# Kernel tuning notes

Hardware: AMD Instinct MI355X
Metric: run time of the kernel (lower is better)

The kernel has to match this reference:

```python
import jax, jax.numpy as jnp
import numpy as np

K = 5            # spline kernel size per dim
NUM_CLASSES = 10
EPS = 1e-4       # matches module's normalize eps
ROUTING_ITERS = 3
_BITS = jnp.array([[(b >> 2) & 1, (b >> 1) & 1, b & 1] for b in range(8)], dtype=jnp.float32)  # [8,3]


def normalize(t, axis=-1):
    return t / (jnp.sqrt(jnp.sum(t * t, axis=axis, keepdims=True)) + EPS)


def quat_mul(q, r):
    # quaternions stored (x, y, z, w) -- module sets identity as [:,:,:,3]=1
    qx, qy, qz, qw = q[..., 0], q[..., 1], q[..., 2], q[..., 3]
    rx, ry, rz, rw = r[..., 0], r[..., 1], r[..., 2], r[..., 3]
    return jnp.stack([
        qw * rx + qx * rw + qy * rz - qz * ry,
        qw * ry - qx * rz + qy * rw + qz * rx,
        qw * rz + qx * ry - qy * rx + qz * rw,
        qw * rw - qx * rx - qy * ry - qz * rz,
    ], axis=-1)


def spline_conv(x, pseudo, src, dst, W, root, bias, n_nodes):
    # degree-1 open B-spline conv, kernel 5^3, in=1, out=16
    v = pseudo * (K - 1)                                   # [E,3]
    i0 = jnp.clip(jnp.floor(v), 0, K - 2)                  # [E,3]
    frac = v - i0
    i0 = i0.astype(jnp.int32)
    idx = i0[:, None, :] + _BITS.astype(jnp.int32)[None]   # [E,8,3]
    kflat = (idx[..., 0] * K + idx[..., 1]) * K + idx[..., 2]  # [E,8]
    wb = jnp.prod(jnp.where(_BITS[None] > 0, frac[:, None, :], 1.0 - frac[:, None, :]), axis=-1)  # [E,8]
    Wg = W[kflat]                                          # [E,8,16] irregular gather (dominant traffic)
    wk = jnp.einsum('eb,ebo->eo', wb, Wg)                  # [E,16]
    msg = x[src] * wk                                      # [E,16] (in-channels = 1)
    agg = jax.ops.segment_sum(msg, dst, num_segments=n_nodes)
    deg = jax.ops.segment_sum(jnp.ones_like(dst, dtype=x.dtype), dst, num_segments=n_nodes)
    return agg / jnp.maximum(deg, 1.0)[:, None] + x @ root + bias


def caps_layer(pose, act, q):
    # pose [N,I,4], act [N,I], q [I,J,4] -> pose [N,J,4], act [N,J]
    qn = normalize(q)
    pred = normalize(quat_mul(qn[None], pose[:, :, None, :]))  # [N,I,J,4]
    b = jnp.zeros(pred.shape[:3], dtype=pose.dtype)
    for _ in range(ROUTING_ITERS):
        c = jax.nn.softmax(b, axis=2) * act[:, :, None]
        s = jnp.einsum('nij,nijq->njq', c, pred)
        v = normalize(s)
        b = b + jnp.einsum('nijq,njq->nij', pred, v)
    act_out = jax.nn.sigmoid(jnp.einsum('nij,nijq,njq->nj', c, pred, v))
    return v, act_out


def pool_by_agreement(pose, act, pos, G, start, size):
    # voxel-grid clustering + agreement-weighted quaternion averaging
    g = jnp.clip(jnp.floor((pos - start) / size), 0, G - 1).astype(jnp.int32)  # [N,3]
    vid = (g[:, 0] * G + g[:, 1]) * G + g[:, 2]
    V = G ** 3
    s = jax.ops.segment_sum(act[:, :, None] * pose, vid, num_segments=V)  # [V,J,4]
    m = normalize(s)
    agree = jnp.sum(pose * m[vid], axis=-1)                                # [N,J]
    wsum = jax.ops.segment_sum(act, vid, num_segments=V)
    cnt = jax.ops.segment_sum(jnp.ones((pose.shape[0],), pose.dtype), vid, num_segments=V)
    act_out = jax.nn.sigmoid(jax.ops.segment_sum(act * agree, vid, num_segments=V) / (wsum + EPS))
    pos_out = jax.ops.segment_sum(pos, vid, num_segments=V) / (cnt[:, None] + EPS)
    return m, act_out, pos_out


def forward(x, pos, pseudo, W_spline, root, bias, lin_w, lin_b, q0, q1, q3, q5, q6, q7, edge_index):
    N = x.shape[0]
    src, dst = edge_index[0], edge_index[1]
    h = spline_conv(x, pseudo, src, dst, W_spline, root, bias, N)   # [N,16]
    quats = jax.nn.elu(h) @ lin_w + lin_b                           # [N,4]
    pose = normalize(quats.reshape(N, 1, 4))                        # [N,1,4]
    act = x.reshape(N, 1)                                           # expand to num_caps_in=1
    pose, act = caps_layer(pose, act, q0)                           # 1 -> 6
    pose, act = caps_layer(pose, act, q1)                           # 6 -> 6
    min_pos, max_pos = pos.min(), pos.max()
    rng = max_pos + 0.001 - min_pos
    pose, act, p = pool_by_agreement(pose, act, pos, 32, min_pos, rng / 32)   # -> 32768 voxels
    pose, act = caps_layer(pose, act, q3)                           # 6 -> 8
    pose, act, p = pool_by_agreement(pose, act, p, 8, min_pos, rng / 8)       # -> 512
    pose, act = caps_layer(pose, act, q5)                           # 8 -> 12
    pose, act, p = pool_by_agreement(pose, act, p, 2, min_pos, rng / 2)       # -> 8
    pose, act = caps_layer(pose, act, q6)                           # 12 -> 14
    pose, act, p = pool_by_agreement(pose, act, p, 1, min_pos - 0.5, max_pos - min_pos + 1.0)  # -> 1
    pose, act = caps_layer(pose, act, q7)                           # 14 -> 10
    return act                                                      # [1, 10]


def setup_inputs() -> dict:
    key = jax.random.key(0)
    ks = jax.random.split(key, 16)
    N, E = 50000, 800000
    def caps_q(k, i, j):
        return jax.random.normal(k, (i, j, 4), dtype=jnp.float32)
    return {
        'x': jax.random.uniform(ks[0], (N, 1), dtype=jnp.float32),
        'pos': jax.random.uniform(ks[1], (N, 3), dtype=jnp.float32),
        'pseudo': jax.random.uniform(ks[2], (E, 3), dtype=jnp.float32),
        'W_spline': jax.random.normal(ks[3], (K ** 3, 16), dtype=jnp.float32) * 0.1,
        'root': jax.random.normal(ks[4], (1, 16), dtype=jnp.float32) * 0.1,
        'bias': jnp.zeros((16,), dtype=jnp.float32),
        'lin_w': jax.random.normal(ks[5], (16, 4), dtype=jnp.float32) * 0.25,
        'lin_b': jnp.zeros((4,), dtype=jnp.float32),
        'q0': caps_q(ks[6], 1, 6),
        'q1': caps_q(ks[7], 6, 6),
        'q3': caps_q(ks[8], 6, 8),
        'q5': caps_q(ks[9], 8, 12),
        'q6': caps_q(ks[10], 12, 14),
        'q7': caps_q(ks[11], 14, NUM_CLASSES),
        'edge_index': jax.random.randint(ks[12], (2, E), 0, N, dtype=jnp.int32),
    }


def reference(x, pos, pseudo, W_spline, root, bias, lin_w, lin_b, q0, q1, q3, q5, q6, q7, edge_index):
    return forward(x, pos, pseudo, W_spline, root, bias, lin_w, lin_b, q0, q1, q3, q5, q6, q7, edge_index)
```

## Files before the change

kernel.cpp:

```cpp
#include <hip/hip_runtime.h>
#include <math.h>

#define EPS 1e-4f

__device__ __forceinline__ float sigmoidf_(float x){ return 1.0f/(1.0f+expf(-x)); }

__device__ __forceinline__ unsigned f2u_(float f){
    unsigned u = __float_as_uint(f);
    return (u & 0x80000000u) ? ~u : (u | 0x80000000u);
}
__device__ __forceinline__ float u2f_(unsigned u){
    unsigned b = (u & 0x80000000u) ? (u & 0x7FFFFFFFu) : ~u;
    return __uint_as_float(b);
}

__global__ void init_kernel(unsigned* __restrict__ mm, int* __restrict__ deg, int N,
                            int* __restrict__ vhead, int V,
                            float* __restrict__ pz, int PZ){
    int i = blockIdx.x*blockDim.x + threadIdx.x;
    int stride = gridDim.x*blockDim.x;
    if (i == 0){ mm[0] = 0xFFFFFFFFu; mm[1] = 0u; }
    for (int t = i; t < N; t += stride) deg[t] = 0;
    for (int t = i; t < V; t += stride) vhead[t] = -1;
    for (int t = i; t < PZ; t += stride) pz[t] = 0.f;
}

__global__ void prep_kernel(const float* __restrict__ p, int n3, unsigned* mm,
                            const int* __restrict__ ei, int* __restrict__ deg,
                            int* __restrict__ rank, int E){
    int gid = blockIdx.x*blockDim.x + threadIdx.x;
    int stride = gridDim.x*blockDim.x;
    float lo = INFINITY, hi = -INFINITY;
    for (int i = gid; i < n3; i += stride){
        float v = p[i]; lo = fminf(lo, v); hi = fmaxf(hi, v);
    }
    for (int off = 32; off > 0; off >>= 1){
        lo = fminf(lo, __shfl_down(lo, off));
        hi = fmaxf(hi, __shfl_down(hi, off));
    }
    __shared__ float slo[4], shi[4];
    int wid = threadIdx.x >> 6;
    if ((threadIdx.x & 63) == 0){ slo[wid] = lo; shi[wid] = hi; }
    __syncthreads();
    if (threadIdx.x == 0){
        for (int w = 1; w < 4; w++){ lo = fminf(lo, slo[w]); hi = fmaxf(hi, shi[w]); }
        atomicMin(&mm[0], f2u_(lo));
        atomicMax(&mm[1], f2u_(hi));
    }
    for (int e = gid; e < E; e += stride)
        rank[e] = atomicAdd(&deg[ei[E + e]], 1);
}

__global__ __launch_bounds__(256)
void scan_bsum(const int* __restrict__ deg, int* __restrict__ bsum, int N){
    int i = blockIdx.x*256 + threadIdx.x;
    int v = (i < N) ? deg[i] : 0;
    for (int o = 32; o > 0; o >>= 1) v += __shfl_down(v, o);
    __shared__ int ws[4];
    if ((threadIdx.x & 63) == 0) ws[threadIdx.x >> 6] = v;
    __syncthreads();
    if (threadIdx.x == 0) bsum[blockIdx.x] = ws[0] + ws[1] + ws[2] + ws[3];
}

__global__ __launch_bounds__(1024)
void scan_top(int* __restrict__ bsum, int NB){
    __shared__ int sh[1024];
    int t = threadIdx.x;
    int v = (t < NB) ? bsum[t] : 0;
    sh[t] = v;
    __syncthreads();
    for (int d = 1; d < 1024; d <<= 1){
        int u = (t >= d) ? sh[t - d] : 0;
        __syncthreads();
        sh[t] += u;
        __syncthreads();
    }
    if (t < NB) bsum[t] = sh[t] - v;
    if (t == 1023) bsum[NB] = sh[1023];
}

__global__ __launch_bounds__(256)
void scan_final(const int* __restrict__ deg, const int* __restrict__ bsum,
                int* __restrict__ off, int N, int NB){
    __shared__ int sh[256];
    int b = blockIdx.x;
    int i = b*256 + threadIdx.x;
    int v = (i < N) ? deg[i] : 0;
    sh[threadIdx.x] = v;
    __syncthreads();
    for (int d = 1; d < 256; d <<= 1){
        int u = (threadIdx.x >= d) ? sh[threadIdx.x - d] : 0;
        __syncthreads();
        sh[threadIdx.x] += u;
        __syncthreads();
    }
    if (i < N) off[i] = bsum[b] + sh[threadIdx.x] - v;
    if (b == 0 && threadIdx.x == 0) off[N] = bsum[NB];
}

__global__ void edge_pack(const int* __restrict__ ei, const float* __restrict__ pseudo,
                          const float* __restrict__ x,
                          const int* __restrict__ rank, const int* __restrict__ off,
                          float4* __restrict__ rec4, int* __restrict__ recb, int E){
    int e = blockIdx.x*blockDim.x + threadIdx.x;
    if (e >= E) return;
    float p0 = pseudo[3*e], p1 = pseudo[3*e+1], p2 = pseudo[3*e+2];
    int s = ei[e], d = ei[E + e];
    float v0 = p0*4.f, v1 = p1*4.f, v2 = p2*4.f;
    float f0 = fminf(fmaxf(floorf(v0), 0.f), 3.f);
    float f1 = fminf(fmaxf(floorf(v1), 0.f), 3.f);
    float f2 = fminf(fmaxf(floorf(v2), 0.f), 3.f);
    int slot = off[d] + rank[e];
    rec4[slot] = make_float4(v0 - f0, v1 - f1, v2 - f2, x[s]);
    recb[slot] = ((int)f0*5 + (int)f1)*5 + (int)f2;
}

__device__ __forceinline__ int voxel_id(const float* __restrict__ pos, int n, int G,
                                        float start, float size){
    int g[3];
    #pragma unroll
    for (int k = 0; k < 3; k++){
        float gg = floorf((pos[(size_t)n*3 + k] - start) / size);
        gg = fminf(fmaxf(gg, 0.f), (float)(G - 1));
        g[k] = (int)gg;
    }
    return (g[0]*G + g[1])*G + g[2];
}

__device__ __forceinline__ void pool_geom(const unsigned* mm, int G, int mode,
                                          float& start, float& size){
    float mn = u2f_(mm[0]), mx = u2f_(mm[1]);
    if (mode == 0){ start = mn; size = (mx + 0.001f - mn) / (float)G; }
    else          { start = mn - 0.5f; size = mx - mn + 1.0f; }
}

__global__ __launch_bounds__(256)
void spline_node_kernel(const float* __restrict__ x, const float4* __restrict__ rec4,
                        const int* __restrict__ recb, const int* __restrict__ off,
                        const float* __restrict__ W,
                        const float* __restrict__ root, const float* __restrict__ bias,
                        const float* __restrict__ lin_w, const float* __restrict__ lin_b,
                        float* __restrict__ pose, float* __restrict__ act, int N){
    __shared__ float Ws[125*17];
    for (int i = threadIdx.x; i < 125*16; i += blockDim.x)
        Ws[(i >> 4)*17 + (i & 15)] = W[i];
    __syncthreads();
    int t = blockIdx.x*blockDim.x + threadIdx.x;
    int n = t >> 3;
    int k = t & 7;
    if (n >= N) return;

    int o0 = off[n], o1 = off[n+1];

    float agg[16];
    #pragma unroll
    for (int o = 0; o < 16; o++) agg[o] = 0.f;

    for (int s = o0 + k; s < o1; s += 8){
        float4 rv = rec4[s];
        int base = recb[s];
        float fr0 = rv.x, fr1 = rv.y, fr2 = rv.z, xv = rv.w;
        #pragma unroll
        for (int b = 0; b < 8; b++){
            int b0 = (b >> 2) & 1, b1 = (b >> 1) & 1, b2 = b & 1;
            float w = (b0 ? fr0 : 1.f - fr0) * (b1 ? fr1 : 1.f - fr1) * (b2 ? fr2 : 1.f - fr2);
            w *= xv;
            const float* Wr = &Ws[(base + b0*25 + b1*5 + b2)*17];
            #pragma unroll
            for (int o = 0; o < 16; o++) agg[o] += w * Wr[o];
        }
    }

    #pragma unroll
    for (int o = 0; o < 16; o++){
        agg[o] += __shfl_xor(agg[o], 1);
        agg[o] += __shfl_xor(agg[o], 2);
        agg[o] += __shfl_xor(agg[o], 4);
    }

    if (k != 0) return;

    float deg = fmaxf((float)(o1 - o0), 1.0f);
    float xs = x[n];
    float qv0 = lin_b[0], qv1 = lin_b[1], qv2 = lin_b[2], qv3 = lin_b[3];
    #pragma unroll
    for (int o = 0; o < 16; o++){
        float h = agg[o] / deg + xs * root[o] + bias[o];
        float e = (h > 0.f) ? h : expm1f(h);
        qv0 += e * lin_w[o*4 + 0];
        qv1 += e * lin_w[o*4 + 1];
        qv2 += e * lin_w[o*4 + 2];
        qv3 += e * lin_w[o*4 + 3];
    }
    float inv = 1.0f / (sqrtf(qv0*qv0 + qv1*qv1 + qv2*qv2 + qv3*qv3) + EPS);
    pose[(size_t)n*4 + 0] = qv0*inv;
    pose[(size_t)n*4 + 1] = qv1*inv;
    pose[(size_t)n*4 + 2] = qv2*inv;
    pose[(size_t)n*4 + 3] = qv3*inv;
    act[n] = xs;
}

__device__ __forceinline__ void quat_pred(const float* qq, float px, float py, float pz,
                                          float pw, float* pr){
    float qx=qq[0], qy=qq[1], qz=qq[2], qw=qq[3];
    float tx = qw*px + qx*pw + qy*pz - qz*py;
    float ty = qw*py - qx*pz + qy*pw + qz*px;
    float tz = qw*pz + qx*py - qy*px + qz*pw;
    float tw = qw*pw - qx*px - qy*py - qz*pz;
    float inv = 1.f/(sqrtf(tx*tx+ty*ty+tz*tz+tw*tw)+EPS);
    pr[0]=tx*inv; pr[1]=ty*inv; pr[2]=tz*inv; pr[3]=tw*inv;
}

template<int I>
__device__ __forceinline__ void caps_route8(const float (*pr)[4], const float* a, bool on,
                                            float* c, float& v0, float& v1,
                                            float& v2, float& v3){
    float b[I];
    #pragma unroll
    for (int i = 0; i < I; i++) b[i] = on ? 0.f : -INFINITY;
    v0=v1=v2=v3=0.f;
    #pragma unroll
    for (int t = 0; t < 3; t++){
        #pragma unroll
        for (int i = 0; i < I; i++){
            float mb = b[i];
            mb = fmaxf(mb, __shfl_xor(mb, 1));
            mb = fmaxf(mb, __shfl_xor(mb, 2));
            mb = fmaxf(mb, __shfl_xor(mb, 4));
            float e = on ? expf(b[i] - mb) : 0.f;
            float s = e;
            s += __shfl_xor(s, 1);
            s += __shfl_xor(s, 2);
            s += __shfl_xor(s, 4);
            c[i] = a[i] * e / s;
        }
        float s0=0.f, s1=0.f, s2=0.f, s3=0.f;
        #pragma unroll
        for (int i = 0; i < I; i++){
            s0 += c[i]*pr[i][0]; s1 += c[i]*pr[i][1];
            s2 += c[i]*pr[i][2]; s3 += c[i]*pr[i][3];
        }
        float inv = 1.f/(sqrtf(s0*s0+s1*s1+s2*s2+s3*s3)+EPS);
        v0=s0*inv; v1=s1*inv; v2=s2*inv; v3=s3*inv;
        if (t < 2){
            #pragma unroll
            for (int i = 0; i < I; i++)
                b[i] += pr[i][0]*v0 + pr[i][1]*v1 + pr[i][2]*v2 + pr[i][3]*v3;
        }
    }
}

__global__ __launch_bounds__(256)
void caps01_kernel(const float* __restrict__ pose0, const float* __restrict__ act0,
                   const float* __restrict__ q0, const float* __restrict__ q1,
                   float* __restrict__ poseOut, float* __restrict__ actOut,
                   const float* __restrict__ pos, int* __restrict__ vhead,
                   int* __restrict__ vnxt, int N, int G,
                   const unsigned* __restrict__ mm){
    __shared__ float qn0[6*4], qn1[36*4];
    for (int t = threadIdx.x; t < 6; t += blockDim.x){
        float qa=q0[t*4],qb=q0[t*4+1],qc=q0[t*4+2],qd=q0[t*4+3];
        float inv=1.f/(sqrtf(qa*qa+qb*qb+qc*qc+qd*qd)+EPS);
        qn0[t*4]=qa*inv; qn0[t*4+1]=qb*inv; qn0[t*4+2]=qc*inv; qn0[t*4+3]=qd*inv;
    }
    for (int t = threadIdx.x; t < 36; t += blockDim.x){
        float qa=q1[t*4],qb=q1[t*4+1],qc=q1[t*4+2],qd=q1[t*4+3];
        float inv=1.f/(sqrtf(qa*qa+qb*qb+qc*qc+qd*qd)+EPS);
        qn1[t*4]=qa*inv; qn1[t*4+1]=qb*inv; qn1[t*4+2]=qc*inv; qn1[t*4+3]=qd*inv;
    }
    __syncthreads();
    int tid = blockIdx.x*blockDim.x + threadIdx.x;
    int n = tid >> 3, j = tid & 7;
    if (n >= N) return;
    bool on = (j < 6);

    float4 p0 = *reinterpret_cast<const float4*>(&pose0[(size_t)n*4]);
    float aa0[1] = { act0[n] };
    float pr0[1][4] = {{0.f,0.f,0.f,0.f}};
    if (on) quat_pred(&qn0[j*4], p0.x, p0.y, p0.z, p0.w, pr0[0]);
    float c0[1], v0x, v0y, v0z, v0w;
    caps_route8<1>(pr0, aa0, on, c0, v0x, v0y, v0z, v0w);
    float al0 = sigmoidf_(c0[0]*(pr0[0][0]*v0x + pr0[0][1]*v0y
                                + pr0[0][2]*v0z + pr0[0][3]*v0w));

    float pi[6][4], ai[6];
    #pragma unroll
    for (int i = 0; i < 6; i++){
        pi[i][0] = __shfl(v0x, i, 8);
        pi[i][1] = __shfl(v0y, i, 8);
        pi[i][2] = __shfl(v0z, i, 8);
        pi[i][3] = __shfl(v0w, i, 8);
        ai[i]    = __shfl(al0, i, 8);
    }

    float pr[6][4];
    #pragma unroll
    for (int i = 0; i < 6; i++){
        pr[i][0]=pr[i][1]=pr[i][2]=pr[i][3]=0.f;
        if (on) quat_pred(&qn1[(i*6+j)*4], pi[i][0], pi[i][1], pi[i][2], pi[i][3], pr[i]);
    }
    float c1[6], v1x, v1y, v1z, v1w;
    caps_route8<6>(pr, ai, on, c1, v1x, v1y, v1z, v1w);
    if (on){
        float acc = 0.f;
        #pragma unroll
        for (int i = 0; i < 6; i++)
            acc += c1[i]*(pr[i][0]*v1x + pr[i][1]*v1y + pr[i][2]*v1z + pr[i][3]*v1w);
        actOut[(size_t)n*6 + j] = sigmoidf_(acc);
        *reinterpret_cast<float4*>(&poseOut[((size_t)n*6 + j)*4]) =
            make_float4(v1x, v1y, v1z, v1w);
    }
    if (j == 0){
        float start, size; pool_geom(mm, G, 0, start, size);
        int vid = voxel_id(pos, n, G, start, size);
        vnxt[n] = atomicExch(&vhead[vid], n);
    }
}

__global__ __launch_bounds__(256)
void pool1caps_kernel(const float* __restrict__ poseIn, const float* __restrict__ actIn,
                      const float* __restrict__ pos,
                      const int* __restrict__ head, const int* __restrict__ nxt,
                      const float* __restrict__ q3,
                      float* __restrict__ poseOut, float* __restrict__ actOut,
                      float* __restrict__ posOut, int V){
    __shared__ float qn[48*4];
    for (int t = threadIdx.x; t < 48; t += blockDim.x){
        float qa=q3[t*4],qb=q3[t*4+1],qc=q3[t*4+2],qd=q3[t*4+3];
        float inv=1.f/(sqrtf(qa*qa+qb*qb+qc*qc+qd*qd)+EPS);
        qn[t*4]=qa*inv; qn[t*4+1]=qb*inv; qn[t*4+2]=qc*inv; qn[t*4+3]=qd*inv;
    }
    __syncthreads();
    int tid = blockIdx.x*blockDim.x + threadIdx.x;
    int v = tid >> 3, j = tid & 7;
    if (v >= V) return;
    bool onj = (j < 6);

    float s0=0.f,s1=0.f,s2=0.f,s3=0.f, w=0.f, ps0=0.f,ps1=0.f,ps2=0.f;
    int cnt = 0;
    for (int n = head[v]; n >= 0; n = nxt[n]){
        if (onj){
            float aj = actIn[(size_t)n*6 + j];
            float4 pb = *reinterpret_cast<const float4*>(&poseIn[((size_t)n*6 + j)*4]);
            s0 += aj*pb.x; s1 += aj*pb.y; s2 += aj*pb.z; s3 += aj*pb.w;
            w += aj;
        } else if (j == 6){
            ps0 += pos[(size_t)n*3+0]; ps1 += pos[(size_t)n*3+1]; ps2 += pos[(size_t)n*3+2];
        }
        cnt++;
    }
    float m0=0.f,m1=0.f,m2=0.f,m3=0.f;
    if (onj){
        float inv = 1.f/(sqrtf(s0*s0+s1*s1+s2*s2+s3*s3)+EPS);
        m0=s0*inv; m1=s1*inv; m2=s2*inv; m3=s3*inv;
    }
    float ag = 0.f;
    for (int n = head[v]; n >= 0; n = nxt[n]){
        if (onj){
            float aj = actIn[(size_t)n*6 + j];
            float4 pb = *reinterpret_cast<const float4*>(&poseIn[((size_t)n*6 + j)*4]);
            ag += aj*(pb.x*m0 + pb.y*m1 + pb.z*m2 + pb.w*m3);
        }
    }
    float actm = sigmoidf_(ag/(w+EPS));
    if (j == 6){
        float c = (float)cnt + EPS;
        posOut[(size_t)v*3+0] = ps0/c;
        posOut[(size_t)v*3+1] = ps1/c;
        posOut[(size_t)v*3+2] = ps2/c;
    }

    float pi[6][4], ai[6];
    #pragma unroll
    for (int i = 0; i < 6; i++){
        pi[i][0] = __shfl(m0, i, 8);
        pi[i][1] = __shfl(m1, i, 8);
        pi[i][2] = __shfl(m2, i, 8);
        pi[i][3] = __shfl(m3, i, 8);
        ai[i]    = __shfl(actm, i, 8);
    }
    float pr[6][4];
    #pragma unroll
    for (int i = 0; i < 6; i++)
        quat_pred(&qn[(i*8+j)*4], pi[i][0], pi[i][1], pi[i][2], pi[i][3], pr[i]);
    float c1[6], vx, vy, vz, vw;
    caps_route8<6>(pr, ai, true, c1, vx, vy, vz, vw);
    float acc = 0.f;
    #pragma unroll
    for (int i = 0; i < 6; i++)
        acc += c1[i]*(pr[i][0]*vx + pr[i][1]*vy + pr[i][2]*vz + pr[i][3]*vw);
    actOut[(size_t)v*8 + j] = sigmoidf_(acc);
    *reinterpret_cast<float4*>(&poseOut[((size_t)v*8 + j)*4]) = make_float4(vx, vy, vz, vw);
}

template<int V, int J, int CH, int NCHUNK>
__global__ void pool_priv1(const float4* __restrict__ poseIn, const float* __restrict__ actIn,
                           const float* __restrict__ posIn,
                           float* __restrict__ s, float* __restrict__ wsum,
                           float* __restrict__ cnt, float* __restrict__ psum,
                           int N, int G, int mode, const unsigned* __restrict__ mm){
    __shared__ float s_[V*CH*4];
    __shared__ float wsum_[V*CH];
    __shared__ float cnt_[V];
    __shared__ float psum_[V*3];
    const int chunk = blockIdx.x % NCHUNK;
    const int slice = blockIdx.x / NCHUNK;
    const int nslices = gridDim.x / NCHUNK;
    const int c0 = chunk * CH;

    for (int t = threadIdx.x; t < V*CH*4; t += blockDim.x) s_[t] = 0.f;
    for (int t = threadIdx.x; t < V*CH; t += blockDim.x) wsum_[t] = 0.f;
    if (chunk == 0){
        for (int t = threadIdx.x; t < V; t += blockDim.x) cnt_[t] = 0.f;
        for (int t = threadIdx.x; t < V*3; t += blockDim.x) psum_[t] = 0.f;
    }
    __syncthreads();

    float start, size; pool_geom(mm, G, mode, start, size);
    int per = (N + nslices - 1) / nslices;
    int n0 = slice * per, n1 = min(N, n0 + per);

    for (int n = n0 + (int)threadIdx.x; n < n1; n += blockDim.x){
        int vid = voxel_id(posIn, n, G, start, size);
        #pragma unroll
        for (int jj = 0; jj < CH; jj++){
            int j = c0 + jj;
            float aj = actIn[(size_t)n*J + j];
            float4 p = poseIn[(size_t)n*J + j];
            int b = (vid*CH + jj)*4;
            atomicAdd(&s_[b+0], aj*p.x);
            atomicAdd(&s_[b+1], aj*p.y);
            atomicAdd(&s_[b+2], aj*p.z);
            atomicAdd(&s_[b+3], aj*p.w);
            atomicAdd(&wsum_[vid*CH + jj], aj);
        }
        if (chunk == 0){
            atomicAdd(&cnt_[vid], 1.0f);
            atomicAdd(&psum_[vid*3+0], posIn[(size_t)n*3+0]);
            atomicAdd(&psum_[vid*3+1], posIn[(size_t)n*3+1]);
            atomicAdd(&psum_[vid*3+2], posIn[(size_t)n*3+2]);
        }
    }
    __syncthreads();

    for (int t = threadIdx.x; t < V*CH*4; t += blockDim.x){
        float val = s_[t];
        if (val != 0.f){
            int v = t / (CH*4), r = t % (CH*4);
            atomicAdd(&s[((size_t)v*J + c0)*4 + r], val);
        }
    }
    for (int t = threadIdx.x; t < V*CH; t += blockDim.x){
        float val = wsum_[t];
        if (val != 0.f){
            int v = t / CH, jj = t % CH;
            atomicAdd(&wsum[(size_t)v*J + c0 + jj], val);
        }
    }
    if (chunk == 0){
        for (int t = threadIdx.x; t < V; t += blockDim.x)
            if (cnt_[t] != 0.f) atomicAdd(&cnt[t], cnt_[t]);
        for (int t = threadIdx.x; t < V*3; t += blockDim.x)
            if (psum_[t] != 0.f) atomicAdd(&psum[t], psum_[t]);
    }
}

template<int V, int J>
__global__ void pool_priv2(const float4* __restrict__ poseIn, const float* __restrict__ actIn,
                           const float* __restrict__ posIn, const float4* __restrict__ m,
                           float* __restrict__ agacc,
                           int N, int G, int mode, const unsigned* __restrict__ mm){
    __shared__ float ag_[V*J];
    for (int t = threadIdx.x; t < V*J; t += blockDim.x) ag_[t] = 0.f;
    __syncthreads();
    float start, size; pool_geom(mm, G, mode, start, size);
    int nslices = gridDim.x;
    int per = (N + nslices - 1) / nslices;
    int n0 = blockIdx.x * per, n1 = min(N, n0 + per);
    for (int n = n0 + (int)threadIdx.x; n < n1; n += blockDim.x){
        int vid = voxel_id(posIn, n, G, start, size);
        #pragma unroll
        for (int j = 0; j < J; j++){
            float4 p  = poseIn[(size_t)n*J + j];
            float4 mv = m[(size_t)vid*J + j];
            float agree = p.x*mv.x + p.y*mv.y + p.z*mv.z + p.w*mv.w;
            atomicAdd(&ag_[vid*J + j], actIn[(size_t)n*J + j]*agree);
        }
    }
    __syncthreads();
    for (int t = threadIdx.x; t < V*J; t += blockDim.x)
        if (ag_[t] != 0.f) atomicAdd(&agacc[t], ag_[t]);
}

__global__ void pool_m2(const float* __restrict__ s, float* __restrict__ m,
                        const float* __restrict__ cnt, const float* __restrict__ psum,
                        float* __restrict__ posOut, int V, int J){
    int t = blockIdx.x*blockDim.x + threadIdx.x;
    if (t < V*J){
        float a = s[(size_t)t*4], b = s[(size_t)t*4+1];
        float c = s[(size_t)t*4+2], d = s[(size_t)t*4+3];
        float inv = 1.0f / (sqrtf(a*a + b*b + c*c + d*d) + EPS);
        m[(size_t)t*4]   = a*inv;
        m[(size_t)t*4+1] = b*inv;
        m[(size_t)t*4+2] = c*inv;
        m[(size_t)t*4+3] = d*inv;
    }
    if (t < V){
        float c = cnt[t] + EPS;
        posOut[(size_t)t*3+0] = psum[(size_t)t*3+0] / c;
        posOut[(size_t)t*3+1] = psum[(size_t)t*3+1] / c;
        posOut[(size_t)t*3+2] = psum[(size_t)t*3+2] / c;
    }
}

template<int I, int J, int NPB>
__global__ __launch_bounds__(NPB*I*J)
void caps_coop_fin(const float* __restrict__ poseIn, const float* __restrict__ agacc,
                   const float* __restrict__ wsum, const float* __restrict__ q,
                   float* __restrict__ poseOut, float* __restrict__ actOut, int N){
    const int IJ = I*J;
    const int tid = threadIdx.x;
    const int nl  = tid / IJ;
    const int li  = tid - nl*IJ;
    const int i   = li / J;
    const int j   = li - i*J;
    const int node = blockIdx.x*NPB + nl;
    const bool on = (node < N);

    __shared__ float redA[NPB][I*J];
    __shared__ float redB[NPB][I*J];
    __shared__ float cp[NPB][I*J*4];
    __shared__ float vsh[NPB][J*4];

    float prx=0.f, pry=0.f, prz=0.f, prw=0.f, ai=0.f;
    if (on){
        float qx = q[li*4+0], qy = q[li*4+1], qz = q[li*4+2], qw = q[li*4+3];
        float qinv = 1.0f/(sqrtf(qx*qx+qy*qy+qz*qz+qw*qw)+EPS);
        qx*=qinv; qy*=qinv; qz*=qinv; qw*=qinv;
        const float* pp = &poseIn[((size_t)node*I + i)*4];
        float rx=pp[0], ry=pp[1], rz=pp[2], rw=pp[3];
        ai = sigmoidf_(agacc[(size_t)node*I + i] / (wsum[(size_t)node*I + i] + EPS));
        float tx = qw*rx + qx*rw + qy*rz - qz*ry;
        float ty = qw*ry - qx*rz + qy*rw + qz*rx;
        float tz = qw*rz + qx*ry - qy*rx + qz*rw;
        float tw = qw*rw - qx*rx - qy*ry - qz*rz;
        float pinv = 1.0f/(sqrtf(tx*tx+ty*ty+tz*tz+tw*tw)+EPS);
        prx=tx*pinv; pry=ty*pinv; prz=tz*pinv; prw=tw*pinv;
    }

    float b = 0.f, c = 0.f;
    for (int t = 0; t < 3; t++){
        redA[nl][li] = b;
        __syncthreads();
        float mb = -INFINITY;
        #pragma unroll
        for (int jj = 0; jj < J; jj++) mb = fmaxf(mb, redA[nl][i*J+jj]);
        float e = expf(b - mb);
        redB[nl][li] = e;
        __syncthreads();
        float s = 0.f;
        #pragma unroll
        for (int jj = 0; jj < J; jj++) s += redB[nl][i*J+jj];
        c = ai * e / s;
        cp[nl][li*4+0] = c*prx; cp[nl][li*4+1] = c*pry;
        cp[nl][li*4+2] = c*prz; cp[nl][li*4+3] = c*prw;
        __syncthreads();
        for (int idx = li; idx < J*4; idx += IJ){
            int jj = idx >> 2, comp = idx & 3;
            float acc = 0.f;
            #pragma unroll
            for (int ii = 0; ii < I; ii++) acc += cp[nl][(ii*J+jj)*4+comp];
            vsh[nl][idx] = acc;
        }
        __syncthreads();
        if (li < J){
            float a0=vsh[nl][li*4], a1=vsh[nl][li*4+1], a2=vsh[nl][li*4+2], a3=vsh[nl][li*4+3];
            float inv = 1.0f/(sqrtf(a0*a0+a1*a1+a2*a2+a3*a3)+EPS);
            vsh[nl][li*4]=a0*inv; vsh[nl][li*4+1]=a1*inv;
            vsh[nl][li*4+2]=a2*inv; vsh[nl][li*4+3]=a3*inv;
        }
        __syncthreads();
        if (t < 2){
            b += prx*vsh[nl][j*4] + pry*vsh[nl][j*4+1] + prz*vsh[nl][j*4+2] + prw*vsh[nl][j*4+3];
            __syncthreads();
        } else {
            redA[nl][li] = c*(prx*vsh[nl][j*4] + pry*vsh[nl][j*4+1]
                            + prz*vsh[nl][j*4+2] + prw*vsh[nl][j*4+3]);
            __syncthreads();
            if (li < J && on){
                float acc = 0.f;
                #pragma unroll
                for (int ii = 0; ii < I; ii++) acc += redA[nl][ii*J+li];
                actOut[(size_t)node*J + li] = sigmoidf_(acc);
                poseOut[((size_t)node*J+li)*4+0] = vsh[nl][li*4+0];
                poseOut[((size_t)node*J+li)*4+1] = vsh[nl][li*4+1];
                poseOut[((size_t)node*J+li)*4+2] = vsh[nl][li*4+2];
                poseOut[((size_t)node*J+li)*4+3] = vsh[nl][li*4+3];
            }
        }
    }
}

__global__ __launch_bounds__(192)
void pool4final_kernel(const float* __restrict__ poseIn, const float* __restrict__ actIn,
                       const float* __restrict__ q7, float* __restrict__ out){
    const int NIN = 8, JP = 14, I = 14, J = 10;
    __shared__ float mp[JP*4], ma[JP];
    __shared__ float redA[I*J], redB[I*J], cp[I*J*4], vsh[J*4];
    int t = threadIdx.x;
    if (t < JP){
        float s0=0.f,s1=0.f,s2=0.f,s3=0.f,w=0.f;
        #pragma unroll
        for (int n = 0; n < NIN; n++){
            float a = actIn[n*JP + t];
            const float* pb = &poseIn[(n*JP + t)*4];
            s0 += a*pb[0]; s1 += a*pb[1]; s2 += a*pb[2]; s3 += a*pb[3];
            w += a;
        }
        float inv = 1.f/(sqrtf(s0*s0+s1*s1+s2*s2+s3*s3)+EPS);
        s0*=inv; s1*=inv; s2*=inv; s3*=inv;
        float ag = 0.f;
        #pragma unroll
        for (int n = 0; n < NIN; n++){
            float a = actIn[n*JP + t];
            const float* pb = &poseIn[(n*JP + t)*4];
            ag += a*(pb[0]*s0 + pb[1]*s1 + pb[2]*s2 + pb[3]*s3);
        }
        ma[t] = sigmoidf_(ag / (w + EPS));
        mp[t*4+0]=s0; mp[t*4+1]=s1; mp[t*4+2]=s2; mp[t*4+3]=s3;
    }
    __syncthreads();

    bool act_thr = (t < I*J);
    int li = act_thr ? t : 0;
    int i = li / J, j = li % J;
    float prx=0.f, pry=0.f, prz=0.f, prw=0.f, ai=0.f;
    if (act_thr){
        float qx=q7[li*4],qy=q7[li*4+1],qz=q7[li*4+2],qw=q7[li*4+3];
        float qinv = 1.f/(sqrtf(qx*qx+qy*qy+qz*qz+qw*qw)+EPS);
        qx*=qinv; qy*=qinv; qz*=qinv; qw*=qinv;
        float rx=mp[i*4], ry=mp[i*4+1], rz=mp[i*4+2], rw=mp[i*4+3];
        ai = ma[i];
        float tx = qw*rx + qx*rw + qy*rz - qz*ry;
        float ty = qw*ry - qx*rz + qy*rw + qz*rx;
        float tz = qw*rz + qx*ry - qy*rx + qz*rw;
        float tw = qw*rw - qx*rx - qy*ry - qz*rz;
        float pinv = 1.f/(sqrtf(tx*tx+ty*ty+tz*tz+tw*tw)+EPS);
        prx=tx*pinv; pry=ty*pinv; prz=tz*pinv; prw=tw*pinv;
    }
    float b = 0.f, c = 0.f;
    for (int it = 0; it < 3; it++){
        if (act_thr) redA[li] = b;
        __syncthreads();
        float mb = -INFINITY;
        #pragma unroll
        for (int jj = 0; jj < J; jj++) mb = fmaxf(mb, redA[i*J+jj]);
        float e = expf(b - mb);
        if (act_thr) redB[li] = e;
        __syncthreads();
        float s = 0.f;
        #pragma unroll
        for (int jj = 0; jj < J; jj++) s += redB[i*J+jj];
        c = ai * e / s;
        if (act_thr){
            cp[li*4+0]=c*prx; cp[li*4+1]=c*pry; cp[li*4+2]=c*prz; cp[li*4+3]=c*prw;
        }
        __syncthreads();
        if (act_thr){
            for (int idx = li; idx < J*4; idx += I*J){
                int jj = idx >> 2, comp = idx & 3;
                float acc = 0.f;
                #pragma unroll
                for (int ii = 0; ii < I; ii++) acc += cp[(ii*J+jj)*4+comp];
                vsh[idx] = acc;
            }
        }
        __syncthreads();
        if (act_thr && li < J){
            float a0=vsh[li*4], a1=vsh[li*4+1], a2=vsh[li*4+2], a3=vsh[li*4+3];
            float inv = 1.f/(sqrtf(a0*a0+a1*a1+a2*a2+a3*a3)+EPS);
            vsh[li*4]=a0*inv; vsh[li*4+1]=a1*inv; vsh[li*4+2]=a2*inv; vsh[li*4+3]=a3*inv;
        }
        __syncthreads();
        if (it < 2){
            b += prx*vsh[j*4] + pry*vsh[j*4+1] + prz*vsh[j*4+2] + prw*vsh[j*4+3];
            __syncthreads();
        } else {
            if (act_thr)
                redA[li] = c*(prx*vsh[j*4] + pry*vsh[j*4+1]
                            + prz*vsh[j*4+2] + prw*vsh[j*4+3]);
            __syncthreads();
            if (act_thr && li < J){
                float acc = 0.f;
                #pragma unroll
                for (int ii = 0; ii < I; ii++) acc += redA[ii*J+li];
                out[li] = sigmoidf_(acc);
            }
        }
    }
}

extern "C" void kernel_launch(void* const* d_in, const int* in_sizes, int n_in,
                              void* d_out, int out_size, void* d_ws, size_t ws_size,
                              hipStream_t stream){
    const float* x      = (const float*)d_in[0];
    const float* pos    = (const float*)d_in[1];
    const float* pseudo = (const float*)d_in[2];
    const float* Wsp    = (const float*)d_in[3];
    const float* root   = (const float*)d_in[4];
    const float* bias   = (const float*)d_in[5];
    const float* lin_w  = (const float*)d_in[6];
    const float* lin_b  = (const float*)d_in[7];
    const float* q0     = (const float*)d_in[8];
    const float* q1     = (const float*)d_in[9];
    const float* q3     = (const float*)d_in[10];
    const float* q5     = (const float*)d_in[11];
    const float* q6     = (const float*)d_in[12];
    const float* q7     = (const float*)d_in[13];
    const int*   ei     = (const int*)d_in[14];
    const int N = in_sizes[0];
    const int E = in_sizes[2] / 3;
    const int V1 = 32768;
    const int NB = (N + 255)/256;

    char* ws = (char*)d_ws;
    size_t off = 0;
    auto alloc = [&](size_t bytes)->void*{
        void* p = ws + off;
        off += (bytes + 255) & ~(size_t)255;
        return p;
    };
    unsigned* mm   = (unsigned*)alloc(8);
    int* deg       = (int*)alloc((size_t)N*sizeof(int));
    int* erank     = (int*)alloc((size_t)E*sizeof(int));
    int* eoff      = (int*)alloc((size_t)(N+1)*sizeof(int));
    int* bsum      = (int*)alloc((size_t)(NB+1)*sizeof(int));
    float4* rec4   = (float4*)alloc((size_t)E*sizeof(float4));
    int* recb      = (int*)alloc((size_t)E*sizeof(int));
    int* vhead     = (int*)alloc((size_t)V1*sizeof(int));
    int* vnxt      = (int*)alloc((size_t)N*sizeof(int));
    float* P0  = (float*)alloc((size_t)1250000*sizeof(float));
    float* P1  = (float*)alloc((size_t)1250000*sizeof(float));
    float* A0  = (float*)alloc((size_t)310000*sizeof(float));
    float* A1  = (float*)alloc((size_t)310000*sizeof(float));
    float* PB0 = (float*)alloc((size_t)100000*sizeof(float));
    float* PB1 = (float*)alloc((size_t)100000*sizeof(float));
    size_t z0 = off;
    float* vs2 = (float*)alloc((size_t)512*8*4*sizeof(float));
    float* vw2 = (float*)alloc((size_t)512*8*sizeof(float));
    float* va2 = (float*)alloc((size_t)512*8*sizeof(float));
    float* vc2 = (float*)alloc((size_t)512*sizeof(float));
    float* vp2 = (float*)alloc((size_t)512*3*sizeof(float));
    float* vs3 = (float*)alloc((size_t)8*12*4*sizeof(float));
    float* vw3 = (float*)alloc((size_t)8*12*sizeof(float));
    float* va3 = (float*)alloc((size_t)8*12*sizeof(float));
    float* vc3 = (float*)alloc((size_t)8*sizeof(float));
    float* vp3 = (float*)alloc((size_t)8*3*sizeof(float));
    size_t z1 = off;
    float* pzero = (float*)(ws + z0);
    const int PZ = (int)((z1 - z0)/sizeof(float));

    init_kernel<<<256, 256, 0, stream>>>(mm, deg, N, vhead, V1, pzero, PZ);
    prep_kernel<<<512, 256, 0, stream>>>(pos, N*3, mm, ei, deg, erank, E);
    scan_bsum<<<NB, 256, 0, stream>>>(deg, bsum, N);
    scan_top<<<1, 1024, 0, stream>>>(bsum, NB);
    scan_final<<<NB, 256, 0, stream>>>(deg, bsum, eoff, N, NB);
    edge_pack<<<(E + 255)/256, 256, 0, stream>>>(ei, pseudo, x, erank, eoff, rec4, recb, E);
    spline_node_kernel<<<(8*N + 255)/256, 256, 0, stream>>>(x, rec4, recb, eoff, Wsp,
                                                            root, bias, lin_w, lin_b, P0, A0, N);

    caps01_kernel<<<(8*N + 255)/256, 256, 0, stream>>>(P0, A0, q0, q1, P1, A1,
                                                       pos, vhead, vnxt, N, 32, mm);
    pool1caps_kernel<<<(8*V1 + 255)/256, 256, 0, stream>>>(P1, A1, pos, vhead, vnxt,
                                                           q3, P0, A0, PB0, V1);

    pool_priv1<512,8,4,2><<<128, 256, 0, stream>>>((const float4*)P0, A0, PB0,
                                                   vs2, vw2, vc2, vp2, 32768, 8, 0, mm);
    pool_m2<<<16, 256, 0, stream>>>(vs2, P1, vc2, vp2, PB1, 512, 8);
    pool_priv2<512,8><<<64, 256, 0, stream>>>((const float4*)P0, A0, PB0,
                                              (const float4*)P1, va2, 32768, 8, 0, mm);
    caps_coop_fin<8,12,2><<<256, 2*96, 0, stream>>>(P1, va2, vw2, q5, P0, A0, 512);

    pool_priv1<8,12,12,1><<<16, 256, 0, stream>>>((const float4*)P0, A0, PB1,
                                                  vs3, vw3, vc3, vp3, 512, 2, 0, mm);
    pool_m2<<<1, 256, 0, stream>>>(vs3, P1, vc3, vp3, PB0, 8, 12);
    pool_priv2<8,12><<<16, 256, 0, stream>>>((const float4*)P0, A0, PB1,
                                             (const float4*)P1, va3, 512, 2, 0, mm);
    caps_coop_fin<12,14,1><<<8, 168, 0, stream>>>(P1, va3, vw3, q6, P0, A0, 8);

    pool4final_kernel<<<1, 192, 0, stream>>>(P0, A0, q7, (float*)d_out);
}
```

Before: 309.3 us.

## Build CSR degrees and edge ranks with per-block LDS histograms over node ranges

Replaces the global-atomic degree count and per-edge rank array with a kernel in which each block owns a 512-node range and counts in-range destinations using LDS atomics. The edge packing kernel rescans all edges per block and assigns slots from a shared-memory counter, which removes the erank buffer and the global atomic contention. The cost is that every block reads the whole destination array, 128 times redundantly. The fixed 128×512 node coverage silently drops nodes if N exceeds 65536.

```diff
diff --git a/kernel.cpp b/kernel.cpp
--- a/kernel.cpp
+++ b/kernel.cpp
@@ -2,6 +2,8 @@
 #include <math.h>
 
 #define EPS 1e-4f
+#define DEGB 128
+#define DRANGE 512
 
 __device__ __forceinline__ float sigmoidf_(float x){ return 1.0f/(1.0f+expf(-x)); }
 
@@ -14,41 +16,53 @@
     return __uint_as_float(b);
 }
 
-__global__ void init_kernel(unsigned* __restrict__ mm, int* __restrict__ deg, int N,
+__global__ void init_kernel(unsigned* __restrict__ mm,
                             int* __restrict__ vhead, int V,
                             float* __restrict__ pz, int PZ){
     int i = blockIdx.x*blockDim.x + threadIdx.x;
     int stride = gridDim.x*blockDim.x;
     if (i == 0){ mm[0] = 0xFFFFFFFFu; mm[1] = 0u; }
-    for (int t = i; t < N; t += stride) deg[t] = 0;
     for (int t = i; t < V; t += stride) vhead[t] = -1;
     for (int t = i; t < PZ; t += stride) pz[t] = 0.f;
 }
 
-__global__ void prep_kernel(const float* __restrict__ p, int n3, unsigned* mm,
-                            const int* __restrict__ ei, int* __restrict__ deg,
-                            int* __restrict__ rank, int E){
-    int gid = blockIdx.x*blockDim.x + threadIdx.x;
-    int stride = gridDim.x*blockDim.x;
+__global__ __launch_bounds__(1024)
+void deg_hist(const float* __restrict__ pos, int n3, unsigned* mm,
+              const int* __restrict__ ei, int* __restrict__ deg, int E, int N){
+    __shared__ int cnt[DRANGE];
+    __shared__ float slo[16], shi[16];
+    for (int t = threadIdx.x; t < DRANGE; t += blockDim.x) cnt[t] = 0;
+
+    int per = (n3 + gridDim.x - 1)/gridDim.x;
+    int p0 = blockIdx.x*per, p1 = min(n3, p0+per);
     float lo = INFINITY, hi = -INFINITY;
-    for (int i = gid; i < n3; i += stride){
-        float v = p[i]; lo = fminf(lo, v); hi = fmaxf(hi, v);
-    }
-    for (int off = 32; off > 0; off >>= 1){
-        lo = fminf(lo, __shfl_down(lo, off));
-        hi = fmaxf(hi, __shfl_down(hi, off));
-    }
-    __shared__ float slo[4], shi[4];
+    for (int i = p0 + (int)threadIdx.x; i < p1; i += blockDim.x){
+        float v = pos[i]; lo = fminf(lo, v); hi = fmaxf(hi, v);
+    }
+    for (int o = 32; o > 0; o >>= 1){
+        lo = fminf(lo, __shfl_down(lo, o));
+        hi = fmaxf(hi, __shfl_down(hi, o));
+    }
     int wid = threadIdx.x >> 6;
     if ((threadIdx.x & 63) == 0){ slo[wid] = lo; shi[wid] = hi; }
     __syncthreads();
     if (threadIdx.x == 0){
-        for (int w = 1; w < 4; w++){ lo = fminf(lo, slo[w]); hi = fmaxf(hi, shi[w]); }
+        for (int w = 1; w < 16; w++){ lo = fminf(lo, slo[w]); hi = fmaxf(hi, shi[w]); }
         atomicMin(&mm[0], f2u_(lo));
         atomicMax(&mm[1], f2u_(hi));
     }
-    for (int e = gid; e < E; e += stride)
-        rank[e] = atomicAdd(&deg[ei[E + e]], 1);
+
+    int base = blockIdx.x * DRANGE;
+    const int* dst = ei + E;
+    for (int e = threadIdx.x; e < E; e += blockDim.x){
+        int d = dst[e] - base;
+        if ((unsigned)d < DRANGE) atomicAdd(&cnt[d], 1);
+    }
+    __syncthreads();
+    for (int t = threadIdx.x; t < DRANGE; t += blockDim.x){
+        int n = base + t;
+        if (n < N) deg[n] = cnt[t];
+    }
 }
 
 __global__ __launch_bounds__(256)
@@ -98,21 +112,31 @@
     if (b == 0 && threadIdx.x == 0) off[N] = bsum[NB];
 }
 
-__global__ void edge_pack(const int* __restrict__ ei, const float* __restrict__ pseudo,
-                          const float* __restrict__ x,
-                          const int* __restrict__ rank, const int* __restrict__ off,
-                          float4* __restrict__ rec4, int* __restrict__ recb, int E){
-    int e = blockIdx.x*blockDim.x + threadIdx.x;
-    if (e >= E) return;
-    float p0 = pseudo[3*e], p1 = pseudo[3*e+1], p2 = pseudo[3*e+2];
-    int s = ei[e], d = ei[E + e];
-    float v0 = p0*4.f, v1 = p1*4.f, v2 = p2*4.f;
-    float f0 = fminf(fmaxf(floorf(v0), 0.f), 3.f);
-    float f1 = fminf(fmaxf(floorf(v1), 0.f), 3.f);
-    float f2 = fminf(fmaxf(floorf(v2), 0.f), 3.f);
-    int slot = off[d] + rank[e];
-    rec4[slot] = make_float4(v0 - f0, v1 - f1, v2 - f2, x[s]);
-    recb[slot] = ((int)f0*5 + (int)f1)*5 + (int)f2;
+__global__ __launch_bounds__(1024)
+void edge_pack2(const int* __restrict__ ei, const float* __restrict__ pseudo,
+                const float* __restrict__ x, const int* __restrict__ eoff,
+                float4* __restrict__ rec4, int* __restrict__ recb, int E, int N){
+    __shared__ int cnt[DRANGE];
+    for (int t = threadIdx.x; t < DRANGE; t += blockDim.x) cnt[t] = 0;
+    __syncthreads();
+    int base = blockIdx.x * DRANGE;
+    const int* dst = ei + E;
+    for (int e = threadIdx.x; e < E; e += blockDim.x){
+        int d = dst[e];
+        int dl = d - base;
+        if ((unsigned)dl < DRANGE){
+            int r = atomicAdd(&cnt[dl], 1);
+            int slot = eoff[d] + r;
+            float p0 = pseudo[3*e], p1 = pseudo[3*e+1], p2 = pseudo[3*e+2];
+            int s = ei[e];
+            float v0 = p0*4.f, v1 = p1*4.f, v2 = p2*4.f;
+            float f0 = fminf(fmaxf(floorf(v0), 0.f), 3.f);
+            float f1 = fminf(fmaxf(floorf(v1), 0.f), 3.f);
+            float f2 = fminf(fmaxf(floorf(v2), 0.f), 3.f);
+            rec4[slot] = make_float4(v0 - f0, v1 - f1, v2 - f2, x[s]);
+            recb[slot] = ((int)f0*5 + (int)f1)*5 + (int)f2;
+        }
+    }
 }
 
 __device__ __forceinline__ int voxel_id(const float* __restrict__ pos, int n, int G,
@@ -732,7 +756,6 @@
     };
     unsigned* mm   = (unsigned*)alloc(8);
     int* deg       = (int*)alloc((size_t)N*sizeof(int));
-    int* erank     = (int*)alloc((size_t)E*sizeof(int));
     int* eoff      = (int*)alloc((size_t)(N+1)*sizeof(int));
     int* bsum      = (int*)alloc((size_t)(NB+1)*sizeof(int));
     float4* rec4   = (float4*)alloc((size_t)E*sizeof(float4));
@@ -760,12 +783,12 @@
     float* pzero = (float*)(ws + z0);
     const int PZ = (int)((z1 - z0)/sizeof(float));
 
-    init_kernel<<<256, 256, 0, stream>>>(mm, deg, N, vhead, V1, pzero, PZ);
-    prep_kernel<<<512, 256, 0, stream>>>(pos, N*3, mm, ei, deg, erank, E);
+    init_kernel<<<128, 256, 0, stream>>>(mm, vhead, V1, pzero, PZ);
+    deg_hist<<<DEGB, 1024, 0, stream>>>(pos, N*3, mm, ei, deg, E, N);
     scan_bsum<<<NB, 256, 0, stream>>>(deg, bsum, N);
     scan_top<<<1, 1024, 0, stream>>>(bsum, NB);
     scan_final<<<NB, 256, 0, stream>>>(deg, bsum, eoff, N, NB);
-    edge_pack<<<(E + 255)/256, 256, 0, stream>>>(ei, pseudo, x, erank, eoff, rec4, recb, E);
+    edge_pack2<<<DEGB, 1024, 0, stream>>>(ei, pseudo, x, eoff, rec4, recb, E, N);
     spline_node_kernel<<<(8*N + 255)/256, 256, 0, stream>>>(x, rec4, recb, eoff, Wsp,
                                                             root, bias, lin_w, lin_b, P0, A0, N);
 
```

Measured after the change: 897.4 us. 2.9x slower.
